# Kernel optimization log

Hardware: AMD Instinct MI355X
Metric: run time of the kernel (lower is better)

Reference implementation:

```python
import jax, jax.numpy as jnp
import numpy as np

B, T, C, H, W = 16, 8, 16, 64, 64
HID = 32          # round(sqrt(num_audio_input_ch * num_latent_ch)) = sqrt(16*64)
LAT = 64          # num_latent_ch
K = 3             # kernel_size


def conv(x, w, b):
    # x: [B,Cin,H,W], w: [Cout,Cin,K,K] (OIHW), SAME padding == padding (1,1) for 3x3
    y = jax.lax.conv_general_dilated(x, w, (1, 1), 'SAME',
                                     dimension_numbers=('NCHW', 'OIHW', 'NCHW'))
    return y + b[None, :, None, None]


def lstm_scan(x_seq, w, b, hid):
    # x_seq: [T,B,Cin,H,W] -> hidden sequence [T,B,hid,H,W]
    Bn, Hh, Ww = x_seq.shape[1], x_seq.shape[3], x_seq.shape[4]
    h0 = jnp.zeros((Bn, hid, Hh, Ww), x_seq.dtype)

    def step(carry, x_t):
        h, c = carry
        z = conv(jnp.concatenate([x_t, h], axis=1), w, b)     # [B,4*hid,H,W]
        i, f, o, g = jnp.split(z, 4, axis=1)                   # gate order i,f,o,g
        c2 = jax.nn.sigmoid(f) * c + jax.nn.sigmoid(i) * jnp.tanh(g)
        h2 = jax.nn.sigmoid(o) * jnp.tanh(c2)
        return (h2, c2), h2

    _, hs = jax.lax.scan(step, (h0, h0), x_seq)
    return hs


def bidir_layer(x_seq, wf, bf, wb, bb, hid):
    hf = lstm_scan(x_seq, wf, bf, hid)
    hb = jnp.flip(lstm_scan(jnp.flip(x_seq, 0), wb, bb, hid), 0)
    return jnp.concatenate([hf, hb], axis=2)                   # [T,B,2*hid,H,W]


def setup_inputs() -> dict:
    key = jax.random.key(0)
    ks = jax.random.split(key, 16)
    s = 0.05
    pe_dim = C * H * W
    inp = {
        'x_audio': jax.random.normal(ks[0], (B, T, C, H, W), jnp.float32),
        'midi_notes': jax.random.uniform(ks[1], (B, T, 2), jnp.float32, 0.0, 127.0),
        # note encoder: Linear(2,4) -> ReLU -> Linear(4, C*H*W) -> Tanh
        'enc_w1': jax.random.normal(ks[2], (2, 4), jnp.float32) * s,
        'enc_b1': jnp.zeros((4,), jnp.float32),
        'enc_w2': jax.random.normal(ks[3], (4, pe_dim), jnp.float32) * s,
        'enc_b2': jnp.zeros((pe_dim,), jnp.float32),
        # layer 0 (input C=16), fwd + bwd cells
        'w0f': jax.random.normal(ks[4], (4 * HID, C + HID, K, K), jnp.float32) * s,
        'b0f': jnp.zeros((4 * HID,), jnp.float32),
        'w0b': jax.random.normal(ks[5], (4 * HID, C + HID, K, K), jnp.float32) * s,
        'b0b': jnp.zeros((4 * HID,), jnp.float32),
        # layer 1 (input 2*HID=64)
        'w1f': jax.random.normal(ks[6], (4 * HID, 2 * HID + HID, K, K), jnp.float32) * s,
        'b1f': jnp.zeros((4 * HID,), jnp.float32),
        'w1b': jax.random.normal(ks[7], (4 * HID, 2 * HID + HID, K, K), jnp.float32) * s,
        'b1b': jnp.zeros((4 * HID,), jnp.float32),
        # final conv: 2*HID -> LAT
        'fc_w': jax.random.normal(ks[8], (LAT, 2 * HID, K, K), jnp.float32) * s,
        'fc_b': jnp.zeros((LAT,), jnp.float32),
    }
    return inp


def reference(x_audio, midi_notes, enc_w1, enc_b1, enc_w2, enc_b2,
              w0f, b0f, w0b, b0b, w1f, b1f, w1b, b1b, fc_w, fc_b):
    # positional encoding from MIDI notes, vectorized over all timesteps
    notes = -0.5 + midi_notes / 64.0                              # [B,T,2]
    pe = jnp.tanh(jax.nn.relu(notes @ enc_w1 + enc_b1) @ enc_w2 + enc_b2)  # [B,T,C*H*W]
    x = x_audio + pe.reshape(x_audio.shape)
    xs = jnp.transpose(x, (1, 0, 2, 3, 4))                        # [T,B,C,H,W]
    h = bidir_layer(xs, w0f, b0f, w0b, b0b, HID)                  # [T,B,64,H,W]
    h = bidir_layer(h, w1f, b1f, w1b, b1b, HID)                   # [T,B,64,H,W]
    return conv(h[-1], fc_w, fc_b)                                # [B,LAT,H,W]
```

## Files before the change

### kernel.cpp

```cpp
#include <hip/hip_runtime.h>

typedef _Float16 f16;
typedef _Float16 f16x8 __attribute__((ext_vector_type(8)));
typedef float f32x16 __attribute__((ext_vector_type(16)));

namespace {

constexpr int B_ = 16, T_ = 8, HW = 4096;

__device__ __forceinline__ float sigm(float x)  { return 1.f / (1.f + __expf(-x)); }
__device__ __forceinline__ float ftanh(float x) { return 1.f - 2.f / (1.f + __expf(2.f * x)); }

__device__ __forceinline__ f32x16 zero16() {
  f32x16 v;
#pragma unroll
  for (int i = 0; i < 16; ++i) v[i] = 0.f;
  return v;
}

__device__ __forceinline__ f16x8 zero8h() {
  f16x8 v;
#pragma unroll
  for (int i = 0; i < 8; ++i) v[i] = (f16)0.f;
  return v;
}

struct WSet { const float* src; f16* dst; int KC, NCO, CIN; };

__global__ void warr_kernel(WSet s0, WSet s1, WSet s2, WSet s3, WSet s4) {
  WSet s = s0;
  switch (blockIdx.y) { case 1: s = s1; break; case 2: s = s2; break;
                        case 3: s = s3; break; case 4: s = s4; break; default: break; }
  int n = 9 * s.KC * s.NCO * 16;
  int i = blockIdx.x * 256 + threadIdx.x;
  if (i >= n) return;
  int kk = i & 15;
  int t = i >> 4;
  int co = t % s.NCO;
  int dkc = t / s.NCO;
  int kc = dkc % s.KC, dydx = dkc / s.KC;
  int ci = kc * 16 + kk;
  float v = (ci < s.CIN) ? s.src[(co * s.CIN + ci) * 9 + dydx] : 0.f;
  s.dst[i] = (f16)v;
}

__global__ void pe_kernel(const float* __restrict__ xa, const float* __restrict__ midi,
                          const float* __restrict__ w1, const float* __restrict__ b1,
                          const float* __restrict__ w2, const float* __restrict__ b2,
                          f16* __restrict__ xs) {
  int gid = blockIdx.x * 256 + threadIdx.x;
  int half = gid & 1;
  int gpx = gid >> 1;
  int bt = gpx >> 12, gp = gpx & 4095;
  float n0 = -0.5f + midi[bt * 2 + 0] * (1.f / 64.f);
  float n1 = -0.5f + midi[bt * 2 + 1] * (1.f / 64.f);
  float hk[4];
#pragma unroll
  for (int k = 0; k < 4; ++k)
    hk[k] = fmaxf(fmaf(n0, w1[k], fmaf(n1, w1[4 + k], b1[k])), 0.f);
  f16x8 ov;
#pragma unroll
  for (int j = 0; j < 8; ++j) {
    int c = half * 8 + j;
    long p = (long)c * HW + gp;
    float z = b2[p];
#pragma unroll
    for (int k = 0; k < 4; ++k) z = fmaf(hk[k], w2[(long)k * 65536 + p], z);
    ov[j] = (f16)(xa[(long)bt * 65536 + p] + ftanh(z));
  }
  *reinterpret_cast<f16x8*>(xs + (long)gpx * 16 + half * 8) = ov;
}

struct ConvDir {
  const f16* x;  long xbs;
  const f16* h;  long hbs;
  const f16* w;
  const float* bias;
  const f16* cin;
  f16* cout;
  float* fout;
  f16* hout; long hobs;
};

template<int CIN1, int CIN2, int CINPAD, int KCF, int KC, int HST, int HOST,
         bool GATES, int NCO>
__global__ __launch_bounds__(256, 2)
void conv_mfma(ConvDir p0, ConvDir p1)
{
  constexpr int NF = NCO / 32;
  constexpr int NPH = 9 * KC;
  constexpr int ACT_BYTES = 180 * CINPAD * 2;
  constexpr int ZB_BYTES  = GATES ? 128 * 128 * 2 : 0;
  constexpr int SMEM = ACT_BYTES > ZB_BYTES ? ACT_BYTES : ZB_BYTES;
  __shared__ __align__(16) char smem[SMEM];
  f16* act = (f16*)smem;
  f16* zls = (f16*)smem;

  const ConvDir P = blockIdx.y ? p1 : p0;
  const int b = blockIdx.z;
  const int tileY = blockIdx.x >> 2, tileX = blockIdx.x & 3;
  const int gy0 = tileY * 8, gx0 = tileX * 16;
  const int tid = threadIdx.x;

  const int lane = tid & 63, wv = tid >> 6;
  const int mg = wv;
  const int rl = lane & 31;
  const int khalf = (lane >> 5) * 8;
  const int laneA = ((rl >> 4) * 18 + (rl & 15)) * CINPAD + khalf;
  const int laneB = rl * 16 + khalf;
  const f16* __restrict__ wng = P.w + laneB;
  const f16* __restrict__ arow = act + laneA;

  constexpr int UPX = CIN1 / 8, UPH = CIN2 / 8, UPP = UPX + UPH;
  constexpr int NU  = 180 * UPP;
  constexpr int PER = (NU + 255) / 256;
  const bool have_h = (P.h != nullptr);
  f16x8 sreg[PER];
#pragma unroll
  for (int p = 0; p < PER; ++p) {
    sreg[p] = zero8h();
    int i = tid + p * 256;
    if (i < NU) {
      int px = i / UPP, u = i - px * UPP;
      int py = px / 18, pxx = px - py * 18;
      int gy = gy0 + py - 1, gx = gx0 + pxx - 1;
      if ((unsigned)gy < 64u && (unsigned)gx < 64u && (u < UPX || have_h)) {
        long gp = (long)gy * 64 + gx;
        const f16* src = (u < UPX) ? (P.x + b * P.xbs + gp * CIN1 + u * 8)
                                   : (P.h + b * P.hbs + gp * HST + (u - UPX) * 8);
        sreg[p] = *reinterpret_cast<const f16x8*>(src);
      }
    }
  }

  f16x8 bfr[3][NF];
  f16x8 afr[2];

  auto LBF = [&](int ph) {
    const int slot = ph % 3;
    const int dydx = ph / KC, kc = ph % KC;
#pragma unroll
    for (int nf = 0; nf < NF; ++nf)
      bfr[slot][nf] = *reinterpret_cast<const f16x8*>(
          wng + ((long)(dydx * KCF + kc) * NCO + nf * 32) * 16);
  };
  auto LAF = [&](int ph) {
    const int slot = ph & 1;
    const int dydx = ph / KC, kc = ph % KC;
    const int dy = dydx / 3, dx = dydx % 3;
    afr[slot] = *reinterpret_cast<const f16x8*>(
        arow + dx * CINPAD + ((mg * 2 + dy) * 18) * CINPAD + kc * 16);
  };

  LBF(0);
  if (NPH > 1) LBF(1);

#pragma unroll
  for (int p = 0; p < PER; ++p) {
    int i = tid + p * 256;
    if (i < NU) {
      int px = i / UPP, u = i - px * UPP;
      *reinterpret_cast<f16x8*>(act + px * CINPAD + u * 8) = sreg[p];
    }
  }
  __syncthreads();

  if (NPH > 2) LBF(2);

  f32x16 acc[NF];
#pragma unroll
  for (int nf = 0; nf < NF; ++nf) acc[nf] = zero16();

  LAF(0);
#pragma unroll
  for (int ph = 0; ph < NPH; ++ph) {
    if (ph + 1 < NPH) LAF(ph + 1);
#pragma unroll
    for (int nf = 0; nf < NF; ++nf)
      acc[nf] = __builtin_amdgcn_mfma_f32_32x32x16_f16(
          afr[ph & 1], bfr[ph % 3][nf], acc[nf], 0, 0, 0);
    if (ph + 3 < NPH) LBF(ph + 3);
  }

  __syncthreads();

  if constexpr (GATES) {
#pragma unroll
    for (int nf = 0; nf < NF; ++nf) {
      const int col = nf * 32 + rl;
      const float bs = P.bias[col];
#pragma unroll
      for (int r = 0; r < 16; ++r) {
        int row = (r & 3) + 8 * (r >> 2) + 4 * (lane >> 5);
        zls[(mg * 32 + row) * 128 + col] = (f16)(acc[nf][r] + bs);
      }
    }
    __syncthreads();
#pragma unroll
    for (int it = 0; it < 2; ++it) {
      const int idx = tid + it * 256;
      const int q = idx & 3, px = idx >> 2;
      const int py = px >> 4, pxx = px & 15;
      const long gp = (long)(gy0 + py) * 64 + (gx0 + pxx);
      const f16* zb = zls + px * 128 + q * 8;
      f16x8 zi8 = *reinterpret_cast<const f16x8*>(zb);
      f16x8 zf8 = *reinterpret_cast<const f16x8*>(zb + 32);
      f16x8 zo8 = *reinterpret_cast<const f16x8*>(zb + 64);
      f16x8 zg8 = *reinterpret_cast<const f16x8*>(zb + 96);
      const long cbase = ((long)b * HW + gp) * 32 + q * 8;
      f16x8 c8 = P.cin ? *reinterpret_cast<const f16x8*>(P.cin + cbase) : zero8h();
      f16x8 c2v, h2v;
#pragma unroll
      for (int j = 0; j < 8; ++j) {
        float c2 = sigm((float)zf8[j]) * (float)c8[j]
                 + sigm((float)zi8[j]) * ftanh((float)zg8[j]);
        c2v[j] = (f16)c2;
        h2v[j] = (f16)(sigm((float)zo8[j]) * ftanh(c2));
      }
      if (P.cout) *reinterpret_cast<f16x8*>(P.cout + cbase) = c2v;
      *reinterpret_cast<f16x8*>(P.hout + b * P.hobs + gp * HOST + q * 8) = h2v;
    }
  } else {
#pragma unroll
    for (int nf = 0; nf < NF; ++nf) {
      const int co = nf * 32 + rl;
      const float bs = P.bias[co];
#pragma unroll
      for (int r = 0; r < 16; ++r) {
        int row = (r & 3) + 8 * (r >> 2) + 4 * (lane >> 5);
        int pxt = mg * 32 + row;
        int py = pxt >> 4, pxx = pxt & 15;
        long gp = (long)(gy0 + py) * 64 + (gx0 + pxx);
        P.fout[((long)b * NCO + co) * HW + gp] = acc[nf][r] + bs;
      }
    }
  }
}

}

extern "C" void kernel_launch(void* const* d_in, const int* in_sizes, int n_in,
                              void* d_out, int out_size, void* d_ws, size_t ws_size,
                              hipStream_t stream) {
  const float* x_audio = (const float*)d_in[0];
  const float* midi    = (const float*)d_in[1];
  const float* enc_w1  = (const float*)d_in[2];
  const float* enc_b1  = (const float*)d_in[3];
  const float* enc_w2  = (const float*)d_in[4];
  const float* enc_b2  = (const float*)d_in[5];
  const float* w0f = (const float*)d_in[6];
  const float* b0f = (const float*)d_in[7];
  const float* w0b = (const float*)d_in[8];
  const float* b0b = (const float*)d_in[9];
  const float* w1f = (const float*)d_in[10];
  const float* b1f = (const float*)d_in[11];
  const float* w1b = (const float*)d_in[12];
  const float* b1b = (const float*)d_in[13];
  const float* fcw = (const float*)d_in[14];
  const float* fcb = (const float*)d_in[15];

  char* ws = (char*)d_ws;
  size_t off = 0;
  auto alloc = [&](size_t bytes) { char* p = ws + off; off += (bytes + 255) & ~(size_t)255; return p; };

  f16* xs    = (f16*)alloc((size_t)B_ * T_ * HW * 16 * 2);
  f16* seq0  = (f16*)alloc((size_t)T_ * B_ * HW * 64 * 2);
  f16* c0f   = (f16*)alloc((size_t)B_ * HW * 32 * 2);
  f16* c0b   = (f16*)alloc((size_t)B_ * HW * 32 * 2);
  f16* c1f   = (f16*)alloc((size_t)B_ * HW * 32 * 2);
  f16* h1p0  = (f16*)alloc((size_t)B_ * HW * 32 * 2);
  f16* h1p1  = (f16*)alloc((size_t)B_ * HW * 32 * 2);
  f16* h1bw  = (f16*)alloc((size_t)B_ * HW * 32 * 2);
  f16* wt0f  = (f16*)alloc((size_t)9 * 3 * 128 * 16 * 2);
  f16* wt0b  = (f16*)alloc((size_t)9 * 3 * 128 * 16 * 2);
  f16* wt1f  = (f16*)alloc((size_t)9 * 6 * 128 * 16 * 2);
  f16* wt1b  = (f16*)alloc((size_t)9 * 6 * 128 * 16 * 2);
  f16* wtfc  = (f16*)alloc((size_t)9 * 4 * 64 * 16 * 2);

  {
    WSet s0{w0f, wt0f, 3, 128, 48}, s1{w0b, wt0b, 3, 128, 48};
    WSet s2{w1f, wt1f, 6, 128, 96}, s3{w1b, wt1b, 6, 128, 96};
    WSet s4{fcw, wtfc, 4, 64, 64};
    warr_kernel<<<dim3(432, 5), 256, 0, stream>>>(s0, s1, s2, s3, s4);
  }

  pe_kernel<<<(B_ * T_ * HW * 2) / 256, 256, 0, stream>>>(
      x_audio, midi, enc_w1, enc_b1, enc_w2, enc_b2, xs);

  const long XSB  = (long)T_ * HW * 16;
  const long SLAB = (long)B_ * HW * 64;
  const long SB   = (long)HW * 64;
  const long HB   = (long)HW * 32;

  dim3 blk(256);

  {
    ConvDir f{xs, XSB, nullptr, SB, wt0f, b0f, nullptr, c0f, nullptr, seq0, SB};
    ConvDir r{xs + (long)7 * HW * 16, XSB, nullptr, SB, wt0b, b0b, nullptr, c0b,
              nullptr, seq0 + (long)7 * SLAB + 32, SB};
    conv_mfma<16, 32, 56, 3, 1, 64, 64, true, 128>
        <<<dim3(32, 2, 16), blk, 0, stream>>>(f, r);
  }
  for (int s = 1; s < 8; ++s) {
    int tf = s, tb = 7 - s;
    ConvDir f{xs + (long)tf * HW * 16, XSB,
              seq0 + (long)(tf - 1) * SLAB, SB,
              wt0f, b0f, c0f, (s == 7) ? nullptr : c0f, nullptr,
              seq0 + (long)tf * SLAB, SB};
    ConvDir r{xs + (long)tb * HW * 16, XSB,
              seq0 + (long)(tb + 1) * SLAB + 32, SB,
              wt0b, b0b, c0b, (s == 7) ? nullptr : c0b, nullptr,
              seq0 + (long)tb * SLAB + 32, SB};
    conv_mfma<16, 32, 56, 3, 3, 64, 64, true, 128>
        <<<dim3(32, 2, 16), blk, 0, stream>>>(f, r);
  }

  {
    ConvDir f{seq0, SB, nullptr, HB, wt1f, b1f, nullptr, c1f, nullptr, h1p0, HB};
    ConvDir r{seq0 + 7 * SLAB, SB, nullptr, HB, wt1b, b1b, nullptr, nullptr, nullptr, h1bw, HB};
    conv_mfma<64, 32, 104, 6, 4, 32, 32, true, 128>
        <<<dim3(32, 2, 16), blk, 0, stream>>>(f, r);
  }
  for (int s = 1; s < 8; ++s) {
    f16* hprev = (s & 1) ? h1p0 : h1p1;
    f16* hcur  = (s & 1) ? h1p1 : h1p0;
    ConvDir f{seq0 + (long)s * SLAB, SB, hprev, HB, wt1f, b1f,
              c1f, (s == 7) ? nullptr : c1f, nullptr, hcur, HB};
    conv_mfma<64, 32, 104, 6, 6, 32, 32, true, 128>
        <<<dim3(32, 1, 16), blk, 0, stream>>>(f, f);
  }

  {
    ConvDir f{h1p1, HB, h1bw, HB, wtfc, fcb, nullptr, nullptr, (float*)d_out, nullptr, 0};
    conv_mfma<32, 32, 72, 4, 4, 32, 32, false, 64>
        <<<dim3(32, 1, 16), blk, 0, stream>>>(f, f);
  }
}
```

Baseline: 510.2 us.

## Split gate output channels across two blocks per tile to double grid parallelism

```diff
diff --git a/kernel.cpp b/kernel.cpp
--- a/kernel.cpp
+++ b/kernel.cpp
@@ -25,7 +25,7 @@
   return v;
 }
 
-struct WSet { const float* src; f16* dst; int KC, NCO, CIN; };
+struct WSet { const float* src; f16* dst; int KC, NCO, CIN, perm; };
 
 __global__ void warr_kernel(WSet s0, WSet s1, WSet s2, WSet s3, WSet s4) {
   WSet s = s0;
@@ -36,9 +36,15 @@
   if (i >= n) return;
   int kk = i & 15;
   int t = i >> 4;
-  int co = t % s.NCO;
+  int cop = t % s.NCO;
   int dkc = t / s.NCO;
   int kc = dkc % s.KC, dydx = dkc / s.KC;
+  int co = cop;
+  if (s.perm) {
+    int hg = cop >> 6, rem = cop & 63;
+    int gate = rem >> 4, h = rem & 15;
+    co = gate * 32 + hg * 16 + h;
+  }
   int ci = kc * 16 + kk;
   float v = (ci < s.CIN) ? s.src[(co * s.CIN + ci) * 9 + dydx] : 0.f;
   s.dst[i] = (f16)v;
@@ -83,14 +89,15 @@
 };
 
 template<int CIN1, int CIN2, int CINPAD, int KCF, int KC, int HST, int HOST,
-         bool GATES, int NCO>
-__global__ __launch_bounds__(256, 2)
+         bool GATES, int NCOT, int CSPL>
+__global__ __launch_bounds__(256, 3)
 void conv_mfma(ConvDir p0, ConvDir p1)
 {
-  constexpr int NF = NCO / 32;
+  constexpr int NB = NCOT / CSPL;
+  constexpr int NF = NB / 32;
   constexpr int NPH = 9 * KC;
   constexpr int ACT_BYTES = 180 * CINPAD * 2;
-  constexpr int ZB_BYTES  = GATES ? 128 * 128 * 2 : 0;
+  constexpr int ZB_BYTES  = GATES ? 128 * NB * 2 : 0;
   constexpr int SMEM = ACT_BYTES > ZB_BYTES ? ACT_BYTES : ZB_BYTES;
   __shared__ __align__(16) char smem[SMEM];
   f16* act = (f16*)smem;
@@ -98,7 +105,10 @@
 
   const ConvDir P = blockIdx.y ? p1 : p0;
   const int b = blockIdx.z;
-  const int tileY = blockIdx.x >> 2, tileX = blockIdx.x & 3;
+  const int bx = blockIdx.x;
+  const int g    = (CSPL == 1) ? 0 : (bx & (CSPL - 1));
+  const int tile = (CSPL == 1) ? bx : (bx >> 1);
+  const int tileY = tile >> 2, tileX = tile & 3;
   const int gy0 = tileY * 8, gx0 = tileX * 16;
   const int tid = threadIdx.x;
 
@@ -108,7 +118,7 @@
   const int khalf = (lane >> 5) * 8;
   const int laneA = ((rl >> 4) * 18 + (rl & 15)) * CINPAD + khalf;
   const int laneB = rl * 16 + khalf;
-  const f16* __restrict__ wng = P.w + laneB;
+  const f16* __restrict__ wng = P.w + laneB + (long)g * NB * 16;
   const f16* __restrict__ arow = act + laneA;
 
   constexpr int UPX = CIN1 / 8, UPH = CIN2 / 8, UPP = UPX + UPH;
@@ -142,7 +152,7 @@
 #pragma unroll
     for (int nf = 0; nf < NF; ++nf)
       bfr[slot][nf] = *reinterpret_cast<const f16x8*>(
-          wng + ((long)(dydx * KCF + kc) * NCO + nf * 32) * 16);
+          wng + ((long)(dydx * KCF + kc) * NCOT + nf * 32) * 16);
   };
   auto LAF = [&](int ph) {
     const int slot = ph & 1;
@@ -188,38 +198,36 @@
 #pragma unroll
     for (int nf = 0; nf < NF; ++nf) {
       const int col = nf * 32 + rl;
-      const float bs = P.bias[col];
+      const int gate = col >> 4, hlo = col & 15;
+      const float bs = P.bias[gate * 32 + g * 16 + hlo];
 #pragma unroll
       for (int r = 0; r < 16; ++r) {
         int row = (r & 3) + 8 * (r >> 2) + 4 * (lane >> 5);
-        zls[(mg * 32 + row) * 128 + col] = (f16)(acc[nf][r] + bs);
+        zls[(mg * 32 + row) * NB + col] = (f16)(acc[nf][r] + bs);
       }
     }
     __syncthreads();
-#pragma unroll
-    for (int it = 0; it < 2; ++it) {
-      const int idx = tid + it * 256;
-      const int q = idx & 3, px = idx >> 2;
-      const int py = px >> 4, pxx = px & 15;
-      const long gp = (long)(gy0 + py) * 64 + (gx0 + pxx);
-      const f16* zb = zls + px * 128 + q * 8;
-      f16x8 zi8 = *reinterpret_cast<const f16x8*>(zb);
-      f16x8 zf8 = *reinterpret_cast<const f16x8*>(zb + 32);
-      f16x8 zo8 = *reinterpret_cast<const f16x8*>(zb + 64);
-      f16x8 zg8 = *reinterpret_cast<const f16x8*>(zb + 96);
-      const long cbase = ((long)b * HW + gp) * 32 + q * 8;
-      f16x8 c8 = P.cin ? *reinterpret_cast<const f16x8*>(P.cin + cbase) : zero8h();
-      f16x8 c2v, h2v;
-#pragma unroll
-      for (int j = 0; j < 8; ++j) {
-        float c2 = sigm((float)zf8[j]) * (float)c8[j]
-                 + sigm((float)zi8[j]) * ftanh((float)zg8[j]);
-        c2v[j] = (f16)c2;
-        h2v[j] = (f16)(sigm((float)zo8[j]) * ftanh(c2));
-      }
-      if (P.cout) *reinterpret_cast<f16x8*>(P.cout + cbase) = c2v;
-      *reinterpret_cast<f16x8*>(P.hout + b * P.hobs + gp * HOST + q * 8) = h2v;
-    }
+    const int q = tid & 1, px = tid >> 1;
+    const int py = px >> 4, pxx = px & 15;
+    const long gp = (long)(gy0 + py) * 64 + (gx0 + pxx);
+    const f16* zb = zls + px * NB + q * 8;
+    f16x8 zi8 = *reinterpret_cast<const f16x8*>(zb);
+    f16x8 zf8 = *reinterpret_cast<const f16x8*>(zb + 16);
+    f16x8 zo8 = *reinterpret_cast<const f16x8*>(zb + 32);
+    f16x8 zg8 = *reinterpret_cast<const f16x8*>(zb + 48);
+    const int ch = g * 16 + q * 8;
+    const long cbase = ((long)b * HW + gp) * 32 + ch;
+    f16x8 c8 = P.cin ? *reinterpret_cast<const f16x8*>(P.cin + cbase) : zero8h();
+    f16x8 c2v, h2v;
+#pragma unroll
+    for (int j = 0; j < 8; ++j) {
+      float c2 = sigm((float)zf8[j]) * (float)c8[j]
+               + sigm((float)zi8[j]) * ftanh((float)zg8[j]);
+      c2v[j] = (f16)c2;
+      h2v[j] = (f16)(sigm((float)zo8[j]) * ftanh(c2));
+    }
+    if (P.cout) *reinterpret_cast<f16x8*>(P.cout + cbase) = c2v;
+    *reinterpret_cast<f16x8*>(P.hout + b * P.hobs + gp * HOST + ch) = h2v;
   } else {
 #pragma unroll
     for (int nf = 0; nf < NF; ++nf) {
@@ -231,7 +239,7 @@
         int pxt = mg * 32 + row;
         int py = pxt >> 4, pxx = pxt & 15;
         long gp = (long)(gy0 + py) * 64 + (gx0 + pxx);
-        P.fout[((long)b * NCO + co) * HW + gp] = acc[nf][r] + bs;
+        P.fout[((long)b * NCOT + co) * HW + gp] = acc[nf][r] + bs;
       }
     }
   }
@@ -278,9 +286,9 @@
   f16* wtfc  = (f16*)alloc((size_t)9 * 4 * 64 * 16 * 2);
 
   {
-    WSet s0{w0f, wt0f, 3, 128, 48}, s1{w0b, wt0b, 3, 128, 48};
-    WSet s2{w1f, wt1f, 6, 128, 96}, s3{w1b, wt1b, 6, 128, 96};
-    WSet s4{fcw, wtfc, 4, 64, 64};
+    WSet s0{w0f, wt0f, 3, 128, 48, 1}, s1{w0b, wt0b, 3, 128, 48, 1};
+    WSet s2{w1f, wt1f, 6, 128, 96, 1}, s3{w1b, wt1b, 6, 128, 96, 1};
+    WSet s4{fcw, wtfc, 4, 64, 64, 0};
     warr_kernel<<<dim3(432, 5), 256, 0, stream>>>(s0, s1, s2, s3, s4);
   }
 
@@ -298,8 +306,8 @@
     ConvDir f{xs, XSB, nullptr, SB, wt0f, b0f, nullptr, c0f, nullptr, seq0, SB};
     ConvDir r{xs + (long)7 * HW * 16, XSB, nullptr, SB, wt0b, b0b, nullptr, c0b,
               nullptr, seq0 + (long)7 * SLAB + 32, SB};
-    conv_mfma<16, 32, 56, 3, 1, 64, 64, true, 128>
-        <<<dim3(32, 2, 16), blk, 0, stream>>>(f, r);
+    conv_mfma<16, 32, 56, 3, 1, 64, 64, true, 128, 2>
+        <<<dim3(64, 2, 16), blk, 0, stream>>>(f, r);
   }
   for (int s = 1; s < 8; ++s) {
     int tf = s, tb = 7 - s;
@@ -311,28 +319,28 @@
               seq0 + (long)(tb + 1) * SLAB + 32, SB,
               wt0b, b0b, c0b, (s == 7) ? nullptr : c0b, nullptr,
               seq0 + (long)tb * SLAB + 32, SB};
-    conv_mfma<16, 32, 56, 3, 3, 64, 64, true, 128>
-        <<<dim3(32, 2, 16), blk, 0, stream>>>(f, r);
+    conv_mfma<16, 32, 56, 3, 3, 64, 64, true, 128, 2>
+        <<<dim3(64, 2, 16), blk, 0, stream>>>(f, r);
   }
 
   {
     ConvDir f{seq0, SB, nullptr, HB, wt1f, b1f, nullptr, c1f, nullptr, h1p0, HB};
     ConvDir r{seq0 + 7 * SLAB, SB, nullptr, HB, wt1b, b1b, nullptr, nullptr, nullptr, h1bw, HB};
-    conv_mfma<64, 32, 104, 6, 4, 32, 32, true, 128>
-        <<<dim3(32, 2, 16), blk, 0, stream>>>(f, r);
+    conv_mfma<64, 32, 104, 6, 4, 32, 32, true, 128, 2>
+        <<<dim3(64, 2, 16), blk, 0, stream>>>(f, r);
   }
   for (int s = 1; s < 8; ++s) {
     f16* hprev = (s & 1) ? h1p0 : h1p1;
     f16* hcur  = (s & 1) ? h1p1 : h1p0;
     ConvDir f{seq0 + (long)s * SLAB, SB, hprev, HB, wt1f, b1f,
               c1f, (s == 7) ? nullptr : c1f, nullptr, hcur, HB};
-    conv_mfma<64, 32, 104, 6, 6, 32, 32, true, 128>
-        <<<dim3(32, 1, 16), blk, 0, stream>>>(f, f);
+    conv_mfma<64, 32, 104, 6, 6, 32, 32, true, 128, 2>
+        <<<dim3(64, 1, 16), blk, 0, stream>>>(f, f);
   }
 
   {
     ConvDir f{h1p1, HB, h1bw, HB, wtfc, fcb, nullptr, nullptr, (float*)d_out, nullptr, 0};
-    conv_mfma<32, 32, 72, 4, 4, 32, 32, false, 64>
+    conv_mfma<32, 32, 72, 4, 4, 32, 32, false, 64, 1>
         <<<dim3(32, 1, 16), blk, 0, stream>>>(f, f);
   }
 }
```

New measurement: 555.2 us. 1.09x slower.
